# Performance work log

Measured on AMD Instinct MI355X. Metric: run time of the kernel, lower is better.

Reference implementation:

```python
import jax, jax.numpy as jnp
import numpy as np

B, T, C = 4, 2048, 1024
H = 16
HD = C // H  # 64


def setup_inputs() -> dict:
    key = jax.random.key(0)
    ks = jax.random.split(key, 5)
    s = 0.02
    return {
        "x": jax.random.normal(ks[0], (B, T, C), jnp.float32),
        "qkv_w": jax.random.normal(ks[1], (3 * C, C), jnp.float32) * s,
        "qkv_b": jax.random.normal(ks[2], (3 * C,), jnp.float32) * s,
        "out_w": jax.random.normal(ks[3], (C, C), jnp.float32) * s,
        "out_b": jax.random.normal(ks[4], (C,), jnp.float32) * s,
    }


def reference(x, qkv_w, qkv_b, out_w, out_b):
    b, t, c = x.shape
    # qkv projection (torch Linear: x @ W^T + b)
    qkv = x @ qkv_w.T + qkv_b                      # (b, t, 3c)
    q, k, v = jnp.split(qkv, 3, axis=-1)
    def rsh(a):
        return a.reshape(b, t, H, HD).transpose(0, 2, 1, 3)  # (b, h, t, hd)
    q, k, v = rsh(q), rsh(k), rsh(v)
    scale = 1.0 / jnp.sqrt(jnp.float32(HD))
    attn = jnp.einsum('bhqd,bhkd->bhqk', q, k) * scale       # (b, h, t, t)
    causal = jnp.tril(jnp.ones((t, t), dtype=bool))
    attn = jnp.where(causal[None, None], attn, -jnp.inf)
    attn = jax.nn.softmax(attn, axis=-1)
    out = jnp.einsum('bhqk,bhkd->bhqd', attn, v)             # (b, h, t, hd)
    out = out.transpose(0, 2, 1, 3).reshape(b, t, c)
    return out @ out_w.T + out_b
```

## Files before the change

### kernel.cpp

```cpp
#include <hip/hip_runtime.h>

typedef __bf16 bf16x8 __attribute__((ext_vector_type(8)));
typedef __bf16 bf16x4 __attribute__((ext_vector_type(4)));
typedef float f32x4 __attribute__((ext_vector_type(4)));

typedef const __attribute__((address_space(1))) void* gptr_t;
typedef __attribute__((address_space(3))) void* lptr_t;

__device__ __forceinline__ f32x4 mfma16(bf16x8 a, bf16x8 b, f32x4 c) {
  return __builtin_amdgcn_mfma_f32_16x16x32_bf16(a, b, c, 0, 0, 0);
}

__device__ __forceinline__ void load_lds16(const __bf16* g, __bf16* l) {
  __builtin_amdgcn_global_load_lds((gptr_t)g, (lptr_t)l, 16, 0, 0);
}

__device__ __forceinline__ float fast_exp2(float x) {
#if __has_builtin(__builtin_amdgcn_exp2f)
  return __builtin_amdgcn_exp2f(x);
#else
  return exp2f(x);
#endif
}

__device__ __forceinline__ unsigned pack_bf16(float f0, float f1) {
  unsigned u0 = __builtin_bit_cast(unsigned, f0) + 0x8000u;
  unsigned u1 = __builtin_bit_cast(unsigned, f1) + 0x8000u;
  return __builtin_amdgcn_perm(u1, u0, 0x07060302);
}

__global__ __launch_bounds__(256) void convert3(
    const float* __restrict__ x, const float* __restrict__ w1,
    const float* __restrict__ w2, __bf16* __restrict__ xb,
    __bf16* __restrict__ w1b, __bf16* __restrict__ w2b) {
  int bid = blockIdx.x;
  const float* src;
  __bf16* dst;
  int base;
  if (bid < 4096) {
    src = x; dst = xb; base = bid;
  } else if (bid < 5632) {
    src = w1; dst = w1b; base = bid - 4096;
  } else {
    src = w2; dst = w2b; base = bid - 5632;
  }
  size_t off = (size_t)base * 2048 + threadIdx.x * 8;
  float4 v0 = *(const float4*)(src + off);
  float4 v1 = *(const float4*)(src + off + 4);
  bf16x8 o = {(__bf16)v0.x, (__bf16)v0.y, (__bf16)v0.z, (__bf16)v0.w,
              (__bf16)v1.x, (__bf16)v1.y, (__bf16)v1.z, (__bf16)v1.w};
  *(bf16x8*)(dst + off) = o;
}

template <bool C_BF16>
__global__ __launch_bounds__(256) void gemm_bt(
    const __bf16* __restrict__ A, const __bf16* __restrict__ B,
    const float* __restrict__ bias, void* __restrict__ Cv, int M, int N,
    int K, int qcols) {
  __shared__ __bf16 As[2][128 * 32];
  __shared__ __bf16 Bs[2][128 * 32];

  const int tid = threadIdx.x;
  const int wid = tid >> 6;
  const int lane = tid & 63;
  const int l15 = lane & 15;
  const int quad = lane >> 4;
  const int bm = blockIdx.y * 128;
  const int bn = blockIdx.x * 128;
  const int wm = (wid & 1) * 64;
  const int wn = (wid >> 1) * 64;

  const int srow = wid * 16 + (lane >> 2);
  const int schunk = ((lane & 3) ^ ((lane >> 3) & 3)) * 8;
  const __bf16* gA = A + (size_t)(bm + srow) * K + schunk;
  const __bf16* gB = B + (size_t)(bn + srow) * K + schunk;
  const int ldsoff = wid * 16 * 32;

  const int fsl = (quad ^ ((l15 >> 1) & 3)) * 8;

  f32x4 acc[4][4] = {};

  load_lds16(gA, &As[0][ldsoff]);
  load_lds16(gA + (size_t)64 * K, &As[0][64 * 32 + ldsoff]);
  load_lds16(gB, &Bs[0][ldsoff]);
  load_lds16(gB + (size_t)64 * K, &Bs[0][64 * 32 + ldsoff]);

  const int niter = K >> 5;
  for (int it = 0; it < niter; ++it) {
    const int cur = it & 1;
    __syncthreads();
    if (it + 1 < niter) {
      int k0 = (it + 1) << 5;
      load_lds16(gA + k0, &As[1 - cur][ldsoff]);
      load_lds16(gA + k0 + (size_t)64 * K, &As[1 - cur][64 * 32 + ldsoff]);
      load_lds16(gB + k0, &Bs[1 - cur][ldsoff]);
      load_lds16(gB + k0 + (size_t)64 * K, &Bs[1 - cur][64 * 32 + ldsoff]);
    }
    bf16x8 af[4], bf[4];
#pragma unroll
    for (int i = 0; i < 4; ++i)
      af[i] = *(const bf16x8*)(&As[cur][(wm + i * 16 + l15) * 32 + fsl]);
#pragma unroll
    for (int i = 0; i < 4; ++i)
      bf[i] = *(const bf16x8*)(&Bs[cur][(wn + i * 16 + l15) * 32 + fsl]);
#pragma unroll
    for (int mt = 0; mt < 4; ++mt)
#pragma unroll
      for (int nt = 0; nt < 4; ++nt)
        acc[mt][nt] = mfma16(af[mt], bf[nt], acc[mt][nt]);
  }

  const float sc = (bn < qcols) ? 0.18033688011112043f : 1.0f;
#pragma unroll
  for (int mt = 0; mt < 4; ++mt) {
#pragma unroll
    for (int nt = 0; nt < 4; ++nt) {
      int gc = bn + wn + nt * 16 + l15;
      float bv = bias[gc];
#pragma unroll
      for (int r = 0; r < 4; ++r) {
        int gr = bm + wm + mt * 16 + quad * 4 + r;
        float val = (acc[mt][nt][r] + bv) * sc;
        if constexpr (C_BF16)
          ((__bf16*)Cv)[(size_t)gr * N + gc] = (__bf16)val;
        else
          ((float*)Cv)[(size_t)gr * N + gc] = val;
      }
    }
  }
}

template <bool MASK>
__device__ __forceinline__ void softmax_block(f32x4 (&s)[2][4],
                                              float (&lsum)[2][4],
                                              __bf16* __restrict__ psw,
                                              int kv0, int qrow_base, int quad,
                                              int l15) {
#pragma unroll
  for (int mt = 0; mt < 2; ++mt) {
#pragma unroll
    for (int r = 0; r < 4; ++r) {
      int prow = mt * 16 + quad * 4 + r;
      float p[4];
#pragma unroll
      for (int nt = 0; nt < 4; ++nt) {
        p[nt] = fast_exp2(s[mt][nt][r]);
        if constexpr (MASK) {
          if ((kv0 + nt * 16 + l15) > (qrow_base + prow)) p[nt] = 0.f;
        }
      }
      lsum[mt][r] += (p[0] + p[1]) + (p[2] + p[3]);
      uint2 w = {pack_bf16(p[0], p[1]), pack_bf16(p[2], p[3])};
      int o = ((l15 >> 1) ^ (prow & 7)) & 7;
      *(uint2*)(psw + prow * 64 + o * 8 + 4 * (l15 & 1)) = w;
    }
  }
}

__global__ __launch_bounds__(256) void attn_kernel(
    const __bf16* __restrict__ qkv, __bf16* __restrict__ out) {
  constexpr int T = 2048, C3 = 3072;
  constexpr int KVSTEP = 64 * C3;
  __shared__ __bf16 Ks[2][64 * 64];
  __shared__ __bf16 Vt[2][64 * 64];
  __shared__ __bf16 Ps[4][32 * 64];

  const int tid = threadIdx.x;
  const int wid = tid >> 6;
  const int lane = tid & 63;
  const int l15 = lane & 15;
  const int quad = lane >> 4;
  const int bh = blockIdx.x;
  const int pb = blockIdx.y;
  const int b = bh >> 4, h = bh & 15;
  const size_t rowbase = (size_t)b * T;

  const int kr = tid >> 3;
  const int kc = tid & 7;
  const int vj = tid >> 4;
  const int vn = tid & 15;

  const __bf16* gk_base = qkv + rowbase * C3 + 1024 + h * 64 + kr * C3 + kc * 8;
  const __bf16* gv_base = qkv + rowbase * C3 + 2048 + h * 64 + vj * C3 + vn * 4;

  int ks_st0 = kr * 64 + ((kc ^ (kr & 7)) * 8);
  int ks_st1 = (kr + 32) * 64 + ((kc ^ ((kr + 32) & 7)) * 8);
  int vt_st[4];
#pragma unroll
  for (int dd = 0; dd < 4; ++dd) {
    int d = 4 * vn + dd;
    vt_st[dd] = d * 64 + ((((vj >> 1) ^ (d & 7) ^ (d >> 3)) & 7) * 8) +
                4 * (vj & 1);
  }
  int kf_off[4][2];
#pragma unroll
  for (int nt = 0; nt < 4; ++nt)
#pragma unroll
    for (int ksi = 0; ksi < 2; ++ksi)
      kf_off[nt][ksi] =
          (nt * 16 + l15) * 64 + (((4 * ksi + quad) ^ (l15 & 7)) * 8);
  int pf_off[2][2];
#pragma unroll
  for (int mt = 0; mt < 2; ++mt)
#pragma unroll
    for (int ksi = 0; ksi < 2; ++ksi)
      pf_off[mt][ksi] =
          (mt * 16 + l15) * 64 + (((4 * ksi + quad) ^ (l15 & 7)) * 8);
  int vf_off[4][2];
#pragma unroll
  for (int ntv = 0; ntv < 4; ++ntv)
#pragma unroll
    for (int ksi = 0; ksi < 2; ++ksi) {
      int d = ntv * 16 + l15;
      vf_off[ntv][ksi] =
          d * 64 + ((((4 * ksi + quad) ^ (d & 7) ^ (d >> 3)) & 7) * 8);
    }

#pragma unroll 1
  for (int phase = 0; phase < 2; ++phase) {
    const int qp = phase == 0 ? pb : 15 - pb;
    const int q0 = qp * 128;
    const int ntiles = 2 * qp + 2;
    const int qrow_base = q0 + wid * 32;

    bf16x8 qf[2][2];
#pragma unroll
    for (int mt = 0; mt < 2; ++mt)
#pragma unroll
      for (int ksi = 0; ksi < 2; ++ksi)
        qf[mt][ksi] = *(const bf16x8*)(
            qkv + (rowbase + qrow_base + mt * 16 + l15) * C3 + h * 64 +
            ksi * 32 + quad * 8);

    f32x4 acc[2][4] = {};
    float lsum[2][4] = {};

    const __bf16* gk = gk_base;
    const __bf16* gv = gv_base;

    bf16x8 kreg[2];
    bf16x4 vreg[4];
    kreg[0] = *(const bf16x8*)(gk);
    kreg[1] = *(const bf16x8*)(gk + 32 * C3);
#pragma unroll
    for (int i = 0; i < 4; ++i)
      vreg[i] = *(const bf16x4*)(gv + i * 16 * C3);

    __syncthreads();

    for (int j = 0; j < ntiles; ++j) {
      __bf16* ksb = Ks[j & 1];
      __bf16* vtb = Vt[j & 1];
      *(bf16x8*)(ksb + ks_st0) = kreg[0];
      *(bf16x8*)(ksb + ks_st1) = kreg[1];
#pragma unroll
      for (int dd = 0; dd < 4; ++dd) {
        bf16x4 t = {vreg[0][dd], vreg[1][dd], vreg[2][dd], vreg[3][dd]};
        *(bf16x4*)(vtb + vt_st[dd]) = t;
      }
      if (j + 1 < ntiles) {
        gk += KVSTEP;
        gv += KVSTEP;
        kreg[0] = *(const bf16x8*)(gk);
        kreg[1] = *(const bf16x8*)(gk + 32 * C3);
#pragma unroll
        for (int i = 0; i < 4; ++i)
          vreg[i] = *(const bf16x4*)(gv + i * 16 * C3);
      }
      __syncthreads();

      const int kv0 = j * 64;
      f32x4 s[2][4] = {};
#pragma unroll
      for (int nt = 0; nt < 4; ++nt) {
#pragma unroll
        for (int ksi = 0; ksi < 2; ++ksi) {
          bf16x8 kf = *(const bf16x8*)(ksb + kf_off[nt][ksi]);
#pragma unroll
          for (int mt = 0; mt < 2; ++mt)
            s[mt][nt] = mfma16(qf[mt][ksi], kf, s[mt][nt]);
        }
      }
      if ((kv0 + 63) > qrow_base)
        softmax_block<true>(s, lsum, Ps[wid], kv0, qrow_base, quad, l15);
      else
        softmax_block<false>(s, lsum, Ps[wid], kv0, qrow_base, quad, l15);

#pragma unroll
      for (int ksi = 0; ksi < 2; ++ksi) {
        bf16x8 pf[2];
#pragma unroll
        for (int mt = 0; mt < 2; ++mt)
          pf[mt] = *(const bf16x8*)(Ps[wid] + pf_off[mt][ksi]);
#pragma unroll
        for (int ntv = 0; ntv < 4; ++ntv) {
          bf16x8 vf = *(const bf16x8*)(vtb + vf_off[ntv][ksi]);
#pragma unroll
          for (int mt = 0; mt < 2; ++mt)
            acc[mt][ntv] = mfma16(pf[mt], vf, acc[mt][ntv]);
        }
      }
    }

#pragma unroll
    for (int mt = 0; mt < 2; ++mt)
#pragma unroll
      for (int r = 0; r < 4; ++r) {
        float l = lsum[mt][r];
        l += __shfl_xor(l, 1);
        l += __shfl_xor(l, 2);
        l += __shfl_xor(l, 4);
        l += __shfl_xor(l, 8);
        float inv = 1.0f / l;
        int row = qrow_base + mt * 16 + quad * 4 + r;
        size_t ob = (rowbase + row) * 1024 + h * 64;
#pragma unroll
        for (int ntv = 0; ntv < 4; ++ntv)
          out[ob + ntv * 16 + l15] = (__bf16)(acc[mt][ntv][r] * inv);
      }
  }
}

extern "C" void kernel_launch(void* const* d_in, const int* in_sizes, int n_in,
                              void* d_out, int out_size, void* d_ws,
                              size_t ws_size, hipStream_t stream) {
  const float* x = (const float*)d_in[0];
  const float* qkv_w = (const float*)d_in[1];
  const float* qkv_b = (const float*)d_in[2];
  const float* out_w = (const float*)d_in[3];
  const float* out_b = (const float*)d_in[4];
  float* out = (float*)d_out;

  __bf16* qkv_ws = (__bf16*)d_ws;
  __bf16* attn_ws = qkv_ws + (size_t)8192 * 3072;
  __bf16* xb = attn_ws + (size_t)8192 * 1024;
  __bf16* wqb = xb + (size_t)8192 * 1024;
  __bf16* wob = wqb + (size_t)3072 * 1024;

  convert3<<<6144, 256, 0, stream>>>(x, qkv_w, out_w, xb, wqb, wob);
  gemm_bt<true><<<dim3(24, 64), 256, 0, stream>>>(xb, wqb, qkv_b, qkv_ws,
                                                  8192, 3072, 1024, 1024);
  attn_kernel<<<dim3(64, 8), 256, 0, stream>>>(qkv_ws, attn_ws);
  gemm_bt<false><<<dim3(8, 64), 256, 0, stream>>>(attn_ws, wob, out_b, out,
                                                  8192, 1024, 1024, 0);
}
```

Baseline: 243.3 us.

## Fuse x fp32-to-bf16 conversion into QKV GEMM and split attention query tiles

The QKV GEMM now reads fp32 x directly, converts it in registers and stores it to LDS after the MFMA loop. This removes the separate x conversion pass and its bf16 round trip through memory. The attention kernel drops its paired two-phase causal load balancing and launches one block per 128-row query tile (16 per head), with heaviest tiles scheduled first. This gives more, unequal blocks and adds a trailing sync per KV tile. Weight conversion now uses the bit-trick packer.

```diff
diff --git a/kernel.cpp b/kernel.cpp
--- a/kernel.cpp
+++ b/kernel.cpp
@@ -29,32 +29,31 @@
   return __builtin_amdgcn_perm(u1, u0, 0x07060302);
 }
 
-__global__ __launch_bounds__(256) void convert3(
-    const float* __restrict__ x, const float* __restrict__ w1,
-    const float* __restrict__ w2, __bf16* __restrict__ xb,
+__device__ __forceinline__ bf16x8 cvt8(float4 v0, float4 v1) {
+  union { bf16x8 h; uint4 u; } r;
+  r.u.x = pack_bf16(v0.x, v0.y);
+  r.u.y = pack_bf16(v0.z, v0.w);
+  r.u.z = pack_bf16(v1.x, v1.y);
+  r.u.w = pack_bf16(v1.z, v1.w);
+  return r.h;
+}
+
+__global__ __launch_bounds__(256) void convert_w(
+    const float* __restrict__ w1, const float* __restrict__ w2,
     __bf16* __restrict__ w1b, __bf16* __restrict__ w2b) {
   int bid = blockIdx.x;
-  const float* src;
-  __bf16* dst;
-  int base;
-  if (bid < 4096) {
-    src = x; dst = xb; base = bid;
-  } else if (bid < 5632) {
-    src = w1; dst = w1b; base = bid - 4096;
-  } else {
-    src = w2; dst = w2b; base = bid - 5632;
-  }
+  const float* src = bid < 1536 ? w1 : w2;
+  __bf16* dst = bid < 1536 ? w1b : w2b;
+  int base = bid < 1536 ? bid : bid - 1536;
   size_t off = (size_t)base * 2048 + threadIdx.x * 8;
   float4 v0 = *(const float4*)(src + off);
   float4 v1 = *(const float4*)(src + off + 4);
-  bf16x8 o = {(__bf16)v0.x, (__bf16)v0.y, (__bf16)v0.z, (__bf16)v0.w,
-              (__bf16)v1.x, (__bf16)v1.y, (__bf16)v1.z, (__bf16)v1.w};
-  *(bf16x8*)(dst + off) = o;
-}
-
-template <bool C_BF16>
+  *(bf16x8*)(dst + off) = cvt8(v0, v1);
+}
+
+template <bool A_F32, bool C_BF16>
 __global__ __launch_bounds__(256) void gemm_bt(
-    const __bf16* __restrict__ A, const __bf16* __restrict__ B,
+    const void* __restrict__ Av, const __bf16* __restrict__ B,
     const float* __restrict__ bias, void* __restrict__ Cv, int M, int N,
     int K, int qcols) {
   __shared__ __bf16 As[2][128 * 32];
@@ -72,16 +71,33 @@
 
   const int srow = wid * 16 + (lane >> 2);
   const int schunk = ((lane & 3) ^ ((lane >> 3) & 3)) * 8;
-  const __bf16* gA = A + (size_t)(bm + srow) * K + schunk;
+  const int ldsoff = wid * 16 * 32;
+  const int ast0 = srow * 32 + (lane & 3) * 8;
+  const int ast1 = (srow + 64) * 32 + (lane & 3) * 8;
+  const int fsl = (quad ^ ((l15 >> 1) & 3)) * 8;
+
   const __bf16* gB = B + (size_t)(bn + srow) * K + schunk;
-  const int ldsoff = wid * 16 * 32;
-
-  const int fsl = (quad ^ ((l15 >> 1) & 3)) * 8;
+  const float* gAf = nullptr;
+  const __bf16* gAh = nullptr;
+  if constexpr (A_F32)
+    gAf = (const float*)Av + (size_t)(bm + srow) * K + schunk;
+  else
+    gAh = (const __bf16*)Av + (size_t)(bm + srow) * K + schunk;
 
   f32x4 acc[4][4] = {};
-
-  load_lds16(gA, &As[0][ldsoff]);
-  load_lds16(gA + (size_t)64 * K, &As[0][64 * 32 + ldsoff]);
+  float4 ar[4];
+
+  if constexpr (A_F32) {
+    ar[0] = *(const float4*)(gAf);
+    ar[1] = *(const float4*)(gAf + 4);
+    ar[2] = *(const float4*)(gAf + (size_t)64 * K);
+    ar[3] = *(const float4*)(gAf + (size_t)64 * K + 4);
+    *(bf16x8*)(&As[0][ast0]) = cvt8(ar[0], ar[1]);
+    *(bf16x8*)(&As[0][ast1]) = cvt8(ar[2], ar[3]);
+  } else {
+    load_lds16(gAh, &As[0][ldsoff]);
+    load_lds16(gAh + (size_t)64 * K, &As[0][64 * 32 + ldsoff]);
+  }
   load_lds16(gB, &Bs[0][ldsoff]);
   load_lds16(gB + (size_t)64 * K, &Bs[0][64 * 32 + ldsoff]);
 
@@ -89,12 +105,20 @@
   for (int it = 0; it < niter; ++it) {
     const int cur = it & 1;
     __syncthreads();
-    if (it + 1 < niter) {
+    const bool more = (it + 1 < niter);
+    if (more) {
       int k0 = (it + 1) << 5;
-      load_lds16(gA + k0, &As[1 - cur][ldsoff]);
-      load_lds16(gA + k0 + (size_t)64 * K, &As[1 - cur][64 * 32 + ldsoff]);
       load_lds16(gB + k0, &Bs[1 - cur][ldsoff]);
       load_lds16(gB + k0 + (size_t)64 * K, &Bs[1 - cur][64 * 32 + ldsoff]);
+      if constexpr (A_F32) {
+        ar[0] = *(const float4*)(gAf + k0);
+        ar[1] = *(const float4*)(gAf + k0 + 4);
+        ar[2] = *(const float4*)(gAf + k0 + (size_t)64 * K);
+        ar[3] = *(const float4*)(gAf + k0 + (size_t)64 * K + 4);
+      } else {
+        load_lds16(gAh + k0, &As[1 - cur][ldsoff]);
+        load_lds16(gAh + k0 + (size_t)64 * K, &As[1 - cur][64 * 32 + ldsoff]);
+      }
     }
     bf16x8 af[4], bf[4];
 #pragma unroll
@@ -108,6 +132,12 @@
 #pragma unroll
       for (int nt = 0; nt < 4; ++nt)
         acc[mt][nt] = mfma16(af[mt], bf[nt], acc[mt][nt]);
+    if constexpr (A_F32) {
+      if (more) {
+        *(bf16x8*)(&As[1 - cur][ast0]) = cvt8(ar[0], ar[1]);
+        *(bf16x8*)(&As[1 - cur][ast1]) = cvt8(ar[2], ar[3]);
+      }
+    }
   }
 
   const float sc = (bn < qcols) ? 0.18033688011112043f : 1.0f;
@@ -171,7 +201,7 @@
   const int l15 = lane & 15;
   const int quad = lane >> 4;
   const int bh = blockIdx.x;
-  const int pb = blockIdx.y;
+  const int qp = 15 - blockIdx.y;
   const int b = bh >> 4, h = bh & 15;
   const size_t rowbase = (size_t)b * T;
 
@@ -180,11 +210,8 @@
   const int vj = tid >> 4;
   const int vn = tid & 15;
 
-  const __bf16* gk_base = qkv + rowbase * C3 + 1024 + h * 64 + kr * C3 + kc * 8;
-  const __bf16* gv_base = qkv + rowbase * C3 + 2048 + h * 64 + vj * C3 + vn * 4;
-
-  int ks_st0 = kr * 64 + ((kc ^ (kr & 7)) * 8);
-  int ks_st1 = (kr + 32) * 64 + ((kc ^ ((kr + 32) & 7)) * 8);
+  const int ks_st0 = kr * 64 + ((kc ^ (kr & 7)) * 8);
+  const int ks_st1 = (kr + 32) * 64 + ((kc ^ ((kr + 32) & 7)) * 8);
   int vt_st[4];
 #pragma unroll
   for (int dd = 0; dd < 4; ++dd) {
@@ -216,109 +243,104 @@
           d * 64 + ((((4 * ksi + quad) ^ (d & 7) ^ (d >> 3)) & 7) * 8);
     }
 
-#pragma unroll 1
-  for (int phase = 0; phase < 2; ++phase) {
-    const int qp = phase == 0 ? pb : 15 - pb;
-    const int q0 = qp * 128;
-    const int ntiles = 2 * qp + 2;
-    const int qrow_base = q0 + wid * 32;
-
-    bf16x8 qf[2][2];
-#pragma unroll
-    for (int mt = 0; mt < 2; ++mt)
-#pragma unroll
-      for (int ksi = 0; ksi < 2; ++ksi)
-        qf[mt][ksi] = *(const bf16x8*)(
-            qkv + (rowbase + qrow_base + mt * 16 + l15) * C3 + h * 64 +
-            ksi * 32 + quad * 8);
-
-    f32x4 acc[2][4] = {};
-    float lsum[2][4] = {};
-
-    const __bf16* gk = gk_base;
-    const __bf16* gv = gv_base;
-
-    bf16x8 kreg[2];
-    bf16x4 vreg[4];
-    kreg[0] = *(const bf16x8*)(gk);
-    kreg[1] = *(const bf16x8*)(gk + 32 * C3);
-#pragma unroll
-    for (int i = 0; i < 4; ++i)
-      vreg[i] = *(const bf16x4*)(gv + i * 16 * C3);
-
+  const int q0 = qp * 128;
+  const int ntiles = 2 * qp + 2;
+  const int qrow_base = q0 + wid * 32;
+
+  bf16x8 qf[2][2];
+#pragma unroll
+  for (int mt = 0; mt < 2; ++mt)
+#pragma unroll
+    for (int ksi = 0; ksi < 2; ++ksi)
+      qf[mt][ksi] = *(const bf16x8*)(
+          qkv + (rowbase + qrow_base + mt * 16 + l15) * C3 + h * 64 +
+          ksi * 32 + quad * 8);
+
+  f32x4 acc[2][4] = {};
+  float lsum[2][4] = {};
+
+  const __bf16* gk = qkv + rowbase * C3 + 1024 + h * 64 + kr * C3 + kc * 8;
+  const __bf16* gv = qkv + rowbase * C3 + 2048 + h * 64 + vj * C3 + vn * 4;
+
+  bf16x8 kreg[2];
+  bf16x4 vreg[4];
+  kreg[0] = *(const bf16x8*)(gk);
+  kreg[1] = *(const bf16x8*)(gk + 32 * C3);
+#pragma unroll
+  for (int i = 0; i < 4; ++i)
+    vreg[i] = *(const bf16x4*)(gv + i * 16 * C3);
+
+  for (int j = 0; j < ntiles; ++j) {
+    __bf16* ksb = Ks[j & 1];
+    __bf16* vtb = Vt[j & 1];
+    *(bf16x8*)(ksb + ks_st0) = kreg[0];
+    *(bf16x8*)(ksb + ks_st1) = kreg[1];
+#pragma unroll
+    for (int dd = 0; dd < 4; ++dd) {
+      bf16x4 t = {vreg[0][dd], vreg[1][dd], vreg[2][dd], vreg[3][dd]};
+      *(bf16x4*)(vtb + vt_st[dd]) = t;
+    }
+    if (j + 1 < ntiles) {
+      gk += KVSTEP;
+      gv += KVSTEP;
+      kreg[0] = *(const bf16x8*)(gk);
+      kreg[1] = *(const bf16x8*)(gk + 32 * C3);
+#pragma unroll
+      for (int i = 0; i < 4; ++i)
+        vreg[i] = *(const bf16x4*)(gv + i * 16 * C3);
+    }
     __syncthreads();
 
-    for (int j = 0; j < ntiles; ++j) {
-      __bf16* ksb = Ks[j & 1];
-      __bf16* vtb = Vt[j & 1];
-      *(bf16x8*)(ksb + ks_st0) = kreg[0];
-      *(bf16x8*)(ksb + ks_st1) = kreg[1];
-#pragma unroll
-      for (int dd = 0; dd < 4; ++dd) {
-        bf16x4 t = {vreg[0][dd], vreg[1][dd], vreg[2][dd], vreg[3][dd]};
-        *(bf16x4*)(vtb + vt_st[dd]) = t;
-      }
-      if (j + 1 < ntiles) {
-        gk += KVSTEP;
-        gv += KVSTEP;
-        kreg[0] = *(const bf16x8*)(gk);
-        kreg[1] = *(const bf16x8*)(gk + 32 * C3);
-#pragma unroll
-        for (int i = 0; i < 4; ++i)
-          vreg[i] = *(const bf16x4*)(gv + i * 16 * C3);
-      }
-      __syncthreads();
-
-      const int kv0 = j * 64;
-      f32x4 s[2][4] = {};
-#pragma unroll
-      for (int nt = 0; nt < 4; ++nt) {
-#pragma unroll
-        for (int ksi = 0; ksi < 2; ++ksi) {
-          bf16x8 kf = *(const bf16x8*)(ksb + kf_off[nt][ksi]);
-#pragma unroll
-          for (int mt = 0; mt < 2; ++mt)
-            s[mt][nt] = mfma16(qf[mt][ksi], kf, s[mt][nt]);
-        }
-      }
-      if ((kv0 + 63) > qrow_base)
-        softmax_block<true>(s, lsum, Ps[wid], kv0, qrow_base, quad, l15);
-      else
-        softmax_block<false>(s, lsum, Ps[wid], kv0, qrow_base, quad, l15);
-
+    const int kv0 = j * 64;
+    f32x4 s[2][4] = {};
+#pragma unroll
+    for (int nt = 0; nt < 4; ++nt) {
 #pragma unroll
       for (int ksi = 0; ksi < 2; ++ksi) {
-        bf16x8 pf[2];
+        bf16x8 kf = *(const bf16x8*)(ksb + kf_off[nt][ksi]);
 #pragma unroll
         for (int mt = 0; mt < 2; ++mt)
-          pf[mt] = *(const bf16x8*)(Ps[wid] + pf_off[mt][ksi]);
-#pragma unroll
-        for (int ntv = 0; ntv < 4; ++ntv) {
-          bf16x8 vf = *(const bf16x8*)(vtb + vf_off[ntv][ksi]);
-#pragma unroll
-          for (int mt = 0; mt < 2; ++mt)
-            acc[mt][ntv] = mfma16(pf[mt], vf, acc[mt][ntv]);
-        }
-      }
-    }
-
-#pragma unroll
-    for (int mt = 0; mt < 2; ++mt)
-#pragma unroll
-      for (int r = 0; r < 4; ++r) {
-        float l = lsum[mt][r];
-        l += __shfl_xor(l, 1);
-        l += __shfl_xor(l, 2);
-        l += __shfl_xor(l, 4);
-        l += __shfl_xor(l, 8);
-        float inv = 1.0f / l;
-        int row = qrow_base + mt * 16 + quad * 4 + r;
-        size_t ob = (rowbase + row) * 1024 + h * 64;
-#pragma unroll
-        for (int ntv = 0; ntv < 4; ++ntv)
-          out[ob + ntv * 16 + l15] = (__bf16)(acc[mt][ntv][r] * inv);
-      }
-  }
+          s[mt][nt] = mfma16(qf[mt][ksi], kf, s[mt][nt]);
+      }
+    }
+    if ((kv0 + 63) > qrow_base)
+      softmax_block<true>(s, lsum, Ps[wid], kv0, qrow_base, quad, l15);
+    else
+      softmax_block<false>(s, lsum, Ps[wid], kv0, qrow_base, quad, l15);
+
+#pragma unroll
+    for (int ksi = 0; ksi < 2; ++ksi) {
+      bf16x8 pf[2];
+#pragma unroll
+      for (int mt = 0; mt < 2; ++mt)
+        pf[mt] = *(const bf16x8*)(Ps[wid] + pf_off[mt][ksi]);
+#pragma unroll
+      for (int ntv = 0; ntv < 4; ++ntv) {
+        bf16x8 vf = *(const bf16x8*)(vtb + vf_off[ntv][ksi]);
+#pragma unroll
+        for (int mt = 0; mt < 2; ++mt)
+          acc[mt][ntv] = mfma16(pf[mt], vf, acc[mt][ntv]);
+      }
+    }
+    __syncthreads();
+  }
+
+#pragma unroll
+  for (int mt = 0; mt < 2; ++mt)
+#pragma unroll
+    for (int r = 0; r < 4; ++r) {
+      float l = lsum[mt][r];
+      l += __shfl_xor(l, 1);
+      l += __shfl_xor(l, 2);
+      l += __shfl_xor(l, 4);
+      l += __shfl_xor(l, 8);
+      float inv = 1.0f / l;
+      int row = qrow_base + mt * 16 + quad * 4 + r;
+      size_t ob = (rowbase + row) * 1024 + h * 64;
+#pragma unroll
+      for (int ntv = 0; ntv < 4; ++ntv)
+        out[ob + ntv * 16 + l15] = (__bf16)(acc[mt][ntv][r] * inv);
+    }
 }
 
 extern "C" void kernel_launch(void* const* d_in, const int* in_sizes, int n_in,
@@ -333,14 +355,13 @@
 
   __bf16* qkv_ws = (__bf16*)d_ws;
   __bf16* attn_ws = qkv_ws + (size_t)8192 * 3072;
-  __bf16* xb = attn_ws + (size_t)8192 * 1024;
-  __bf16* wqb = xb + (size_t)8192 * 1024;
+  __bf16* wqb = attn_ws + (size_t)8192 * 1024;
   __bf16* wob = wqb + (size_t)3072 * 1024;
 
-  convert3<<<6144, 256, 0, stream>>>(x, qkv_w, out_w, xb, wqb, wob);
-  gemm_bt<true><<<dim3(24, 64), 256, 0, stream>>>(xb, wqb, qkv_b, qkv_ws,
-                                                  8192, 3072, 1024, 1024);
-  attn_kernel<<<dim3(64, 8), 256, 0, stream>>>(qkv_ws, attn_ws);
-  gemm_bt<false><<<dim3(8, 64), 256, 0, stream>>>(attn_ws, wob, out_b, out,
-                                                  8192, 1024, 1024, 0);
-}
+  convert_w<<<2048, 256, 0, stream>>>(qkv_w, out_w, wqb, wob);
+  gemm_bt<true, true><<<dim3(24, 64), 256, 0, stream>>>(
+      x, wqb, qkv_b, qkv_ws, 8192, 3072, 1024, 1024);
+  attn_kernel<<<dim3(64, 16), 256, 0, stream>>>(qkv_ws, attn_ws);
+  gemm_bt<false, false><<<dim3(8, 64), 256, 0, stream>>>(
+      attn_ws, wob, out_b, out, 8192, 1024, 1024, 0);
+}
```

Result: slower. 263.8 us (+8.4%).
